# Kernel optimization log

Hardware: AMD Instinct MI355X
Metric: run time of the kernel (lower is better)

The kernel has to match this reference:

```python
import jax, jax.numpy as jnp
import numpy as np

N, D, K = 32768, 256, 8192
SQRT3 = 3.0 ** 0.5


def setup_inputs() -> dict:
    key = jax.random.key(0)
    k1, k2 = jax.random.split(key)
    x = jax.random.normal(k1, (N, D), dtype=jnp.float32)
    # torch .uniform_(-sqrt(3), sqrt(3)) on an [D, K] table
    embeddings = jax.random.uniform(k2, (D, K), dtype=jnp.float32,
                                    minval=-SQRT3, maxval=SQRT3)
    return {"x": x, "embeddings": embeddings}


def reference(x, embeddings):
    # x: [N, D] (forward flattens from dim 1; 2D input is identity)
    # embeddings: [D, K]
    # squared L2 distances: ||y||^2 - 2 y.E + ||e||^2  -> [N, K]
    dist = (jnp.sum(x * x, axis=1, keepdims=True)
            - 2.0 * (x @ embeddings)
            + jnp.sum(embeddings * embeddings, axis=0, keepdims=True))
    idx = jnp.argmin(dist, axis=1)  # [N]
    # one_hot(idx) @ E^T == gather of columns of E (same math, no dense one-hot)
    quantized = jnp.take(embeddings, idx, axis=1).T  # [N, D]
    return quantized.reshape(x.shape)
```

## Files before the change

kernel.cpp:

```cpp
#include <hip/hip_runtime.h>
#include <math.h>
#include <float.h>

#define N_ROWS 32768
#define D_DIM  256
#define K_DIM  8192

#define EPS1 0.25f
#define EPS2 0.02f
#define T2CAP 4096
#define NSPLIT2 32
#define T3CAP 512
#define NSPLIT3 16

typedef _Float16 f16;
typedef _Float16 f16x8 __attribute__((ext_vector_type(8)));
typedef float f32x4 __attribute__((ext_vector_type(4)));

#define KSPLIT 8
#define COLS_PER_SPLIT (K_DIM / KSPLIT)
#define CHUNK_COLS 32
#define NCHUNK (COLS_PER_SPLIT / CHUNK_COLS)
#define CHUNK_BYTES (CHUNK_COLS * D_DIM * 2)

typedef unsigned int u32;
typedef const u32 __attribute__((address_space(1)))* gas1_u32;
typedef u32 __attribute__((address_space(3)))* las3_u32;
__device__ __forceinline__ void gload_lds16(const void* g, void* l) {
    __builtin_amdgcn_global_load_lds((gas1_u32)g, (las3_u32)l, 16, 0, 0);
}

__global__ void convx_kernel(const float* __restrict__ X, f16* __restrict__ X16,
                             int* __restrict__ count, int* __restrict__ count3) {
    if (blockIdx.x == 0 && threadIdx.x == 0) { *count = 0; *count3 = 0; }
    const size_t i = ((size_t)blockIdx.x * 256 + threadIdx.x) * 8;
    float4 a = *reinterpret_cast<const float4*>(X + i);
    float4 b = *reinterpret_cast<const float4*>(X + i + 4);
    f16x8 o;
    o[0]=(f16)a.x; o[1]=(f16)a.y; o[2]=(f16)a.z; o[3]=(f16)a.w;
    o[4]=(f16)b.x; o[5]=(f16)b.y; o[6]=(f16)b.z; o[7]=(f16)b.w;
    *reinterpret_cast<f16x8*>(X16 + i) = o;
}

__global__ void prep_e_kernel(const float* __restrict__ E, float* __restrict__ ET,
                              f16* __restrict__ Epack) {
    __shared__ float t[64][65];
    const int bk = blockIdx.x & (K_DIM / 64 - 1);
    const int bd = blockIdx.x >> 7;
    const int c  = threadIdx.x & 63;
    const int r0 = (threadIdx.x >> 6) * 16;
    const int d0 = bd * 64, k0 = bk * 64;
#pragma unroll
    for (int i = 0; i < 16; ++i)
        t[r0 + i][c] = E[(size_t)(d0 + r0 + i) * K_DIM + k0 + c];
    __syncthreads();
#pragma unroll
    for (int i = 0; i < 16; ++i)
        ET[(size_t)(k0 + r0 + i) * D_DIM + d0 + c] = t[c][r0 + i];
#pragma unroll
    for (int o = 0; o < 2; ++o) {
        const int out = threadIdx.x + o * 256;
        const int i16 = out >> 7;
        const int th  = (out >> 6) & 1;
        const int l   = out & 63;
        const int tile = bk * 4 + i16;
        const int tg   = bd * 2 + th;
        f16x8 frag;
#pragma unroll
        for (int j = 0; j < 8; ++j)
            frag[j] = (f16)t[32*th + (l >> 4) * 8 + j][16*i16 + (l & 15)];
        *reinterpret_cast<f16x8*>(Epack + ((size_t)(tile*8 + tg) * 512 + l * 8)) = frag;
    }
}

__global__ void packe_kernel(const float* __restrict__ E, f16* __restrict__ Epack) {
    const int gid = blockIdx.x * 256 + threadIdx.x;
    const int l    = gid & 63;
    const int t    = (gid >> 6) & 7;
    const int tile = gid >> 9;
    const int k  = 16 * tile + (l & 15);
    const int d0 = 32 * t + (l >> 4) * 8;
    f16x8 o;
#pragma unroll
    for (int j = 0; j < 8; ++j) o[j] = (f16)E[(size_t)(d0 + j) * K_DIM + k];
    *reinterpret_cast<f16x8*>(Epack + (size_t)gid * 8) = o;
}

__global__ void nhen_kernel(const float* __restrict__ E, float* __restrict__ nhen) {
    const int k = blockIdx.x * 256 + threadIdx.x;
    float s = 0.0f;
#pragma unroll 8
    for (int d = 0; d < D_DIM; ++d) {
        float v = E[(size_t)d * K_DIM + k];
        s = fmaf(v, v, s);
    }
    nhen[k] = -0.5f * s;
}

__launch_bounds__(256, 2)
__global__ void pass1_kernel(const f16* __restrict__ X16,
                             const f16* __restrict__ Epack,
                             const float* __restrict__ nhen,
                             float* __restrict__ p_best,
                             float* __restrict__ p_sec,
                             int*   __restrict__ p_idx) {
    __shared__ f16 B_lds[3][CHUNK_BYTES / 2];
    __shared__ float nh_lds[COLS_PER_SPLIT];

    const int tid = threadIdx.x;
    const int wv = tid >> 6;
    const int lane = tid & 63;
    const int l15 = lane & 15;
    const int l4  = lane >> 4;
    const int rg = blockIdx.x >> 3;
    const int ks = blockIdx.x & 7;
    const int rowW = rg * 256 + wv * 64;
    const int colBase = ks * COLS_PER_SPLIT;

    f16x8 A[4][8];
#pragma unroll
    for (int rt = 0; rt < 4; ++rt)
#pragma unroll
        for (int t = 0; t < 8; ++t)
            A[rt][t] = *reinterpret_cast<const f16x8*>(
                X16 + (size_t)(rowW + 16*rt + l15) * D_DIM + 32*t + l4*8);

    *reinterpret_cast<float4*>(&nh_lds[tid * 4]) =
        *reinterpret_cast<const float4*>(nhen + colBase + tid * 4);

    float best[16], sec[16];
    int bbase[16];
#pragma unroll
    for (int s = 0; s < 16; ++s) { best[s] = -INFINITY; sec[s] = -INFINITY; bbase[s] = 0; }

    const char* splitSrc = (const char*)Epack + (size_t)colBase * 512;

    auto STAGE = [&](int buf, int ci) {
        const char* csrc = splitSrc + (size_t)ci * CHUNK_BYTES;
        char* cdst = (char*)&B_lds[buf][0];
#pragma unroll
        for (int c = 0; c < 4; ++c) {
            const int seg = wv * 4 + c;
            gload_lds16(csrc + seg * 1024 + (lane << 4), cdst + seg * 1024);
        }
    };

    f32x4 accA[4], accB[4];
    int cA = 0, cB = 0;

    auto TILE = [&](const f16* bufc, int ct, int nhoff,
                    f32x4 (&accN)[4], f32x4 (&accP)[4], int cP, bool doScore) {
        const float nh = nh_lds[nhoff + l15];
        const f32x4 nh4 = {nh, nh, nh, nh};
#pragma unroll
        for (int t = 0; t < 8; ++t) {
            f16x8 B = *reinterpret_cast<const f16x8*>(bufc + (ct*8 + t)*512 + lane*8);
            if (t == 0) {
#pragma unroll
                for (int rt = 0; rt < 4; ++rt)
                    accN[rt] = __builtin_amdgcn_mfma_f32_16x16x32_f16(A[rt][0], B, nh4, 0, 0, 0);
            } else {
#pragma unroll
                for (int rt = 0; rt < 4; ++rt)
                    accN[rt] = __builtin_amdgcn_mfma_f32_16x16x32_f16(A[rt][t], B, accN[rt], 0, 0, 0);
            }
            if (doScore) {
#pragma unroll
                for (int s = 2*t; s <= 2*t + 1; ++s) {
                    const int rt2 = s >> 2, r2 = s & 3;
                    const float v = accP[rt2][r2];
                    sec[s] = __builtin_amdgcn_fmed3f(v, best[s], sec[s]);
                    const bool gt = v > best[s];
                    best[s] = gt ? v : best[s];
                    bbase[s] = gt ? cP : bbase[s];
                }
            }
        }
    };

    STAGE(0, 0);
    STAGE(1, 1);
    asm volatile("s_waitcnt lgkmcnt(0)" ::: "memory");

    int cur = 0;
    for (int ci = 0; ci < NCHUNK; ++ci) {
        if (ci < NCHUNK - 1) {
            asm volatile("s_waitcnt vmcnt(4)" ::: "memory");
        } else {
            asm volatile("s_waitcnt vmcnt(0)" ::: "memory");
        }
        __builtin_amdgcn_s_barrier();
        if (ci + 2 < NCHUNK) {
            int nb = cur + 2; if (nb >= 3) nb -= 3;
            STAGE(nb, ci + 2);
        }
        const f16* bufc = &B_lds[cur][0];
        const int base = colBase + ci * CHUNK_COLS;
        if (ci == 0) {
            TILE(bufc, 0, ci*32,      accA, accB, cB, false); cA = base;
            TILE(bufc, 1, ci*32 + 16, accB, accA, cA, true);  cB = base + 16;
        } else {
            TILE(bufc, 0, ci*32,      accA, accB, cB, true);  cA = base;
            TILE(bufc, 1, ci*32 + 16, accB, accA, cA, true);  cB = base + 16;
        }
        cur = (cur + 1 == 3) ? 0 : cur + 1;
    }
#pragma unroll
    for (int s = 0; s < 16; ++s) {
        const int rt2 = s >> 2, r2 = s & 3;
        const float v = accB[rt2][r2];
        sec[s] = __builtin_amdgcn_fmed3f(v, best[s], sec[s]);
        const bool gt = v > best[s];
        best[s] = gt ? v : best[s];
        bbase[s] = gt ? cB : bbase[s];
    }

#pragma unroll
    for (int s = 0; s < 16; ++s) {
        float b = best[s], sc = sec[s];
        int k = bbase[s] + l15;
#pragma unroll
        for (int off = 8; off >= 1; off >>= 1) {
            float ob = __shfl_xor(b, off, 16);
            float os = __shfl_xor(sc, off, 16);
            int   ok = __shfl_xor(k, off, 16);
            float sm = fmaxf(fmaxf(sc, os), fminf(b, ob));
            bool take = (ob > b) || (ob == b && ok < k);
            b = take ? ob : b;
            k = take ? ok : k;
            sc = sm;
        }
        if (l15 == 0) {
            const int row = rowW + 16*(s >> 2) + 4*l4 + (s & 3);
            p_best[ks * N_ROWS + row] = b;
            p_sec [ks * N_ROWS + row] = sc;
            p_idx [ks * N_ROWS + row] = k;
        }
    }
}

__global__ void merge_kernel(const float* __restrict__ p_best,
                             const float* __restrict__ p_sec,
                             const int*   __restrict__ p_idx,
                             int* __restrict__ idxf,
                             int* __restrict__ list, int* __restrict__ count) {
    const int n = blockIdx.x * 256 + threadIdx.x;
    float b = p_best[n], sc = p_sec[n];
    int k = p_idx[n];
#pragma unroll
    for (int s = 1; s < KSPLIT; ++s) {
        float ob = p_best[s * N_ROWS + n];
        float os = p_sec [s * N_ROWS + n];
        int   ok = p_idx [s * N_ROWS + n];
        float sm = fmaxf(fmaxf(sc, os), fminf(b, ob));
        bool take = ob > b;
        b = take ? ob : b; k = take ? ok : k; sc = sm;
    }
    idxf[n] = k;
    if (2.0f * (b - sc) < EPS1) {
        int pos = atomicAdd(count, 1);
        if (pos < T2CAP) list[pos] = n;
    }
}

__launch_bounds__(256, 2)
__global__ void tier2_kernel(const float* __restrict__ X,
                             const float* __restrict__ E,
                             const float* __restrict__ nhen,
                             const int* __restrict__ list,
                             const int* __restrict__ count,
                             float* __restrict__ t2b, float* __restrict__ t2s,
                             int* __restrict__ t2i) {
    const int g  = blockIdx.x >> 5;
    const int sp = blockIdx.x & 31;
    const int cnt = min(*count, T2CAP);
    if (g * 64 >= cnt) return;

    __shared__ float xT[D_DIM][64];
    __shared__ float es[64][64];
    const int tid = threadIdx.x;
    const int tx = tid & 15, ty = tid >> 4;

    {
        const int r = tid >> 2;
        const int slot = min(g * 64 + r, cnt - 1);
        const int row = list[slot];
        const int d0 = (tid & 3) * 64;
        const float* xp = X + (size_t)row * D_DIM + d0;
#pragma unroll
        for (int i = 0; i < 64; i += 4) {
            float4 v = *reinterpret_cast<const float4*>(xp + i);
            xT[d0+i+0][r] = v.x; xT[d0+i+1][r] = v.y;
            xT[d0+i+2][r] = v.z; xT[d0+i+3][r] = v.w;
        }
    }

    float best[4], sec[4]; int bidx[4];
#pragma unroll
    for (int i = 0; i < 4; ++i) { best[i] = -INFINITY; sec[i] = -INFINITY; bidx[i] = 0; }

    const int colBase = sp * 256;
    for (int kc = 0; kc < 256; kc += 64) {
        float acc[4][4];
#pragma unroll
        for (int i = 0; i < 4; ++i)
#pragma unroll
            for (int j = 0; j < 4; ++j) acc[i][j] = 0.0f;

        for (int dc = 0; dc < D_DIM; dc += 64) {
            __syncthreads();
#pragma unroll
            for (int dd = 0; dd < 64; dd += 16) {
                int d = dd + (tid >> 4);
                float4 v = *reinterpret_cast<const float4*>(
                    &E[(size_t)(dc + d) * K_DIM + colBase + kc + (tid & 15) * 4]);
                *reinterpret_cast<float4*>(&es[d][(tid & 15) * 4]) = v;
            }
            __syncthreads();
#pragma unroll 8
            for (int d = 0; d < 64; ++d) {
                float4 xv = *reinterpret_cast<const float4*>(&xT[dc + d][ty * 4]);
                float4 ev = *reinterpret_cast<const float4*>(&es[d][tx * 4]);
                float xr[4] = {xv.x, xv.y, xv.z, xv.w};
                float ec[4] = {ev.x, ev.y, ev.z, ev.w};
#pragma unroll
                for (int i = 0; i < 4; ++i)
#pragma unroll
                    for (int j = 0; j < 4; ++j)
                        acc[i][j] = fmaf(xr[i], ec[j], acc[i][j]);
            }
        }
        float4 nhv = *reinterpret_cast<const float4*>(&nhen[colBase + kc + tx * 4]);
        float nh[4] = {nhv.x, nhv.y, nhv.z, nhv.w};
#pragma unroll
        for (int j = 0; j < 4; ++j) {
            const int k = colBase + kc + tx * 4 + j;
#pragma unroll
            for (int i = 0; i < 4; ++i) {
                float u = nh[j] + acc[i][j];
                bool gt = u > best[i];
                sec[i]  = fmaxf(sec[i], fminf(u, best[i]));
                best[i] = gt ? u : best[i];
                bidx[i] = gt ? k : bidx[i];
            }
        }
    }

#pragma unroll
    for (int off = 8; off >= 1; off >>= 1) {
#pragma unroll
        for (int i = 0; i < 4; ++i) {
            float ob = __shfl_xor(best[i], off, 16);
            float os = __shfl_xor(sec[i], off, 16);
            int   ok = __shfl_xor(bidx[i], off, 16);
            float sm = fmaxf(fmaxf(sec[i], os), fminf(best[i], ob));
            bool take = (ob > best[i]) || (ob == best[i] && ok < bidx[i]);
            best[i] = take ? ob : best[i];
            bidx[i] = take ? ok : bidx[i];
            sec[i] = sm;
        }
    }
    if (tx == 0) {
#pragma unroll
        for (int i = 0; i < 4; ++i) {
            const int slot = g * 64 + ty * 4 + i;
            if (slot < cnt) {
                t2b[sp * T2CAP + slot] = best[i];
                t2s[sp * T2CAP + slot] = sec[i];
                t2i[sp * T2CAP + slot] = bidx[i];
            }
        }
    }
}

__global__ void merge2_kernel(const float* __restrict__ t2b,
                              const float* __restrict__ t2s,
                              const int*   __restrict__ t2i,
                              const int* __restrict__ list,
                              const int* __restrict__ count,
                              int* __restrict__ idxf,
                              int* __restrict__ list3, int* __restrict__ count3) {
    const int slot = blockIdx.x * 256 + threadIdx.x;
    const int cnt = min(*count, T2CAP);
    if (slot >= cnt) return;
    float b = t2b[slot], sc = t2s[slot];
    int k = t2i[slot];
#pragma unroll
    for (int sp = 1; sp < NSPLIT2; ++sp) {
        float ob = t2b[sp * T2CAP + slot];
        float os = t2s[sp * T2CAP + slot];
        int   ok = t2i[sp * T2CAP + slot];
        float sm = fmaxf(fmaxf(sc, os), fminf(b, ob));
        bool take = ob > b;
        b = take ? ob : b; k = take ? ok : k; sc = sm;
    }
    const int n = list[slot];
    idxf[n] = k;
    if (2.0f * (b - sc) < EPS2) {
        int pos = atomicAdd(count3, 1);
        if (pos < T3CAP) list3[pos] = n;
    }
}

__launch_bounds__(256)
__global__ void tier3_kernel(const float* __restrict__ X,
                             const float* __restrict__ E,
                             const int* __restrict__ list3,
                             const int* __restrict__ count3,
                             double* __restrict__ t3b, int* __restrict__ t3i) {
    const int slot = blockIdx.x >> 4;
    const int sp   = blockIdx.x & 15;
    const int cnt = min(*count3, T3CAP);
    if (slot >= cnt) return;
    const int n = list3[slot];

    __shared__ float xs[D_DIM];
    const int tid = threadIdx.x;
    xs[tid] = X[(size_t)n * D_DIM + tid];
    __syncthreads();

    const int colBase = sp * 512;
    double best = DBL_MAX;
    int bi = 0x7fffffff;
#pragma unroll
    for (int kk = 0; kk < 512; kk += 256) {
        const int k = colBase + kk + tid;
        double s0 = 0.0, s1 = 0.0, s2 = 0.0, s3 = 0.0;
#pragma unroll 4
        for (int d = 0; d < D_DIM; d += 4) {
            double f0 = (double)xs[d+0] - (double)E[(size_t)(d+0) * K_DIM + k];
            double f1 = (double)xs[d+1] - (double)E[(size_t)(d+1) * K_DIM + k];
            double f2 = (double)xs[d+2] - (double)E[(size_t)(d+2) * K_DIM + k];
            double f3 = (double)xs[d+3] - (double)E[(size_t)(d+3) * K_DIM + k];
            s0 = fma(f0, f0, s0); s1 = fma(f1, f1, s1);
            s2 = fma(f2, f2, s2); s3 = fma(f3, f3, s3);
        }
        double s = (s0 + s1) + (s2 + s3);
        if (s < best) { best = s; bi = k; }
    }

    __shared__ double bv[256];
    __shared__ int bix[256];
    bv[tid] = best; bix[tid] = bi;
    __syncthreads();
    if (tid == 0) {
        double b = bv[0]; int ix = bix[0];
        for (int t = 1; t < 256; ++t)
            if (bv[t] < b || (bv[t] == b && bix[t] < ix)) { b = bv[t]; ix = bix[t]; }
        t3b[sp * T3CAP + slot] = b;
        t3i[sp * T3CAP + slot] = ix;
    }
}

__global__ void merge3_kernel(const double* __restrict__ t3b,
                              const int* __restrict__ t3i,
                              const int* __restrict__ list3,
                              const int* __restrict__ count3,
                              int* __restrict__ idxf) {
    const int slot = blockIdx.x * 256 + threadIdx.x;
    const int cnt = min(*count3, T3CAP);
    if (slot >= cnt) return;
    double b = t3b[slot];
    int k = t3i[slot];
#pragma unroll
    for (int sp = 1; sp < NSPLIT3; ++sp) {
        double ob = t3b[sp * T3CAP + slot];
        int   ok = t3i[sp * T3CAP + slot];
        if (ob < b || (ob == b && ok < k)) { b = ob; k = ok; }
    }
    idxf[list3[slot]] = k;
}

__global__ void gather2_kernel(const float* __restrict__ ET,
                               const int* __restrict__ idx,
                               float* __restrict__ out) {
    const int n  = blockIdx.x * 4 + (threadIdx.x >> 6);
    const int d4 = (threadIdx.x & 63) * 4;
    const int k  = idx[n];
    *reinterpret_cast<float4*>(&out[(size_t)n * D_DIM + d4]) =
        *reinterpret_cast<const float4*>(&ET[(size_t)k * D_DIM + d4]);
}

__global__ void gather_kernel(const float* __restrict__ E,
                              const int* __restrict__ idx,
                              float* __restrict__ out) {
    const int n = blockIdx.x;
    const int d = threadIdx.x;
    const int k = idx[n];
    out[(size_t)n * D_DIM + d] = E[(size_t)d * K_DIM + k];
}

__global__ void fb_enorm_kernel(const float* __restrict__ E, float* __restrict__ enorm) {
    int k = blockIdx.x * 256 + threadIdx.x;
    float s = 0.0f;
#pragma unroll 8
    for (int d = 0; d < D_DIM; ++d) { float v = E[(size_t)d * K_DIM + k]; s = fmaf(v, v, s); }
    enorm[k] = s;
}

__launch_bounds__(256, 2)
__global__ void fb_dist_kernel(const float* __restrict__ X, const float* __restrict__ E,
                               const float* __restrict__ enorm,
                               int* __restrict__ idx_out, float* __restrict__ gap_out) {
    __shared__ float xT[D_DIM][64];
    __shared__ float es[64][64];
    const int tid = threadIdx.x;
    const int tx = tid & 15, ty = tid >> 4;
    const int rowBase = blockIdx.x * 64;
    {
        const int r = tid >> 2;
        const int d0 = (tid & 3) * 64;
        const float* xp = X + (size_t)(rowBase + r) * D_DIM + d0;
#pragma unroll
        for (int i = 0; i < 64; i += 4) {
            float4 v = *reinterpret_cast<const float4*>(xp + i);
            xT[d0+i+0][r]=v.x; xT[d0+i+1][r]=v.y; xT[d0+i+2][r]=v.z; xT[d0+i+3][r]=v.w;
        }
    }
    float bestVal[4], secVal[4]; int bestIdx[4];
#pragma unroll
    for (int i = 0; i < 4; ++i) { bestVal[i]=INFINITY; secVal[i]=INFINITY; bestIdx[i]=0; }
    for (int kc = 0; kc < K_DIM; kc += 64) {
        float acc[4][4];
#pragma unroll
        for (int i=0;i<4;++i)
#pragma unroll
            for (int j=0;j<4;++j) acc[i][j]=0.f;
        for (int dc = 0; dc < D_DIM; dc += 64) {
            __syncthreads();
#pragma unroll
            for (int dd = 0; dd < 64; dd += 16) {
                int d = dd + (tid >> 4);
                float4 v = *reinterpret_cast<const float4*>(
                    &E[(size_t)(dc+d)*K_DIM + kc + (tid&15)*4]);
                *reinterpret_cast<float4*>(&es[d][(tid&15)*4]) = v;
            }
            __syncthreads();
#pragma unroll 8
            for (int d = 0; d < 64; ++d) {
                float4 xv = *reinterpret_cast<const float4*>(&xT[dc+d][ty*4]);
                float4 ev = *reinterpret_cast<const float4*>(&es[d][tx*4]);
                float xr[4]={xv.x,xv.y,xv.z,xv.w}, ec[4]={ev.x,ev.y,ev.z,ev.w};
#pragma unroll
                for (int i=0;i<4;++i)
#pragma unroll
                    for (int j=0;j<4;++j) acc[i][j]=fmaf(xr[i],ec[j],acc[i][j]);
            }
        }
        float4 env = *reinterpret_cast<const float4*>(&enorm[kc + tx*4]);
        float en[4]={env.x,env.y,env.z,env.w};
#pragma unroll
        for (int j=0;j<4;++j) {
            int k = kc + tx*4 + j;
#pragma unroll
            for (int i=0;i<4;++i) {
                float s = fmaf(-2.0f, acc[i][j], en[j]);
                if (s < bestVal[i]) { secVal[i]=bestVal[i]; bestVal[i]=s; bestIdx[i]=k; }
                else if (s < secVal[i]) secVal[i]=s;
            }
        }
    }
#pragma unroll
    for (int off=8; off>=1; off>>=1) {
#pragma unroll
        for (int i=0;i<4;++i) {
            float oB=__shfl_xor(bestVal[i],off,16);
            int oI=__shfl_xor(bestIdx[i],off,16);
            float oS=__shfl_xor(secVal[i],off,16);
            float ms=fminf(fminf(secVal[i],oS),fmaxf(bestVal[i],oB));
            if (oB<bestVal[i] || (oB==bestVal[i] && oI<bestIdx[i])) { bestVal[i]=oB; bestIdx[i]=oI; }
            secVal[i]=ms;
        }
    }
    if (tx==0) {
#pragma unroll
        for (int i=0;i<4;++i) {
            idx_out[rowBase + ty*4 + i] = bestIdx[i];
            gap_out[rowBase + ty*4 + i] = secVal[i]-bestVal[i];
        }
    }
}

__launch_bounds__(256)
__global__ void fb_refine_kernel(const float* __restrict__ X, const float* __restrict__ E,
                                 const float* __restrict__ gap, int* __restrict__ idx) {
    const int n = blockIdx.x;
    if (gap[n] >= 0.0625f) return;
    __shared__ float xs[D_DIM];
    const int tid = threadIdx.x;
    xs[tid] = X[(size_t)n * D_DIM + tid];
    __syncthreads();
    double best = DBL_MAX; int bi = 0x7fffffff;
    for (int k = tid; k < K_DIM; k += 256) {
        double s0=0,s1=0,s2=0,s3=0;
#pragma unroll 4
        for (int d = 0; d < D_DIM; d += 4) {
            double f0=(double)xs[d+0]-(double)E[(size_t)(d+0)*K_DIM+k];
            double f1=(double)xs[d+1]-(double)E[(size_t)(d+1)*K_DIM+k];
            double f2=(double)xs[d+2]-(double)E[(size_t)(d+2)*K_DIM+k];
            double f3=(double)xs[d+3]-(double)E[(size_t)(d+3)*K_DIM+k];
            s0=fma(f0,f0,s0); s1=fma(f1,f1,s1); s2=fma(f2,f2,s2); s3=fma(f3,f3,s3);
        }
        double s=(s0+s1)+(s2+s3);
        if (s<best){best=s;bi=k;}
    }
    __shared__ double bv[256]; __shared__ int bix[256];
    bv[tid]=best; bix[tid]=bi;
    __syncthreads();
    if (tid==0) {
        double b=bv[0]; int ix=bix[0];
        for (int t=1;t<256;++t)
            if (bv[t]<b || (bv[t]==b && bix[t]<ix)) { b=bv[t]; ix=bix[t]; }
        idx[n]=ix;
    }
}

extern "C" void kernel_launch(void* const* d_in, const int* in_sizes, int n_in,
                              void* d_out, int out_size, void* d_ws, size_t ws_size,
                              hipStream_t stream) {
    const float* X = (const float*)d_in[0];
    const float* E = (const float*)d_in[1];
    float* out = (float*)d_out;
    char* ws = (char*)d_ws;

    const size_t o_nhen  = 0;
    const size_t o_pb    = 32768;
    const size_t o_ps    = o_pb  + (size_t)KSPLIT * N_ROWS * 4;
    const size_t o_pi    = o_ps  + (size_t)KSPLIT * N_ROWS * 4;
    const size_t o_idx   = o_pi  + (size_t)KSPLIT * N_ROWS * 4;
    const size_t o_list  = o_idx + (size_t)N_ROWS * 4;
    const size_t o_count = o_list + (size_t)T2CAP * 4;
    const size_t o_t2b   = o_count + 256;
    const size_t o_t2s   = o_t2b + (size_t)NSPLIT2 * T2CAP * 4;
    const size_t o_t2i   = o_t2s + (size_t)NSPLIT2 * T2CAP * 4;
    const size_t o_list3 = o_t2i + (size_t)NSPLIT2 * T2CAP * 4;
    const size_t o_t3b   = o_list3 + (size_t)T3CAP * 4;
    const size_t o_t3i   = o_t3b + (size_t)NSPLIT3 * T3CAP * 8;
    const size_t o_x16   = o_t3i + (size_t)NSPLIT3 * T3CAP * 4;
    const size_t o_epack = o_x16 + (size_t)N_ROWS * D_DIM * 2;
    const size_t NEED_BASE = o_epack + (size_t)D_DIM * K_DIM * 2;
    const size_t o_et    = NEED_BASE;
    const size_t NEED_FULL = o_et + (size_t)D_DIM * K_DIM * 4;

    if (ws_size >= NEED_BASE) {
        float*  nhen  = (float*) (ws + o_nhen);
        float*  p_b   = (float*) (ws + o_pb);
        float*  p_s   = (float*) (ws + o_ps);
        int*    p_i   = (int*)   (ws + o_pi);
        int*    idxf  = (int*)   (ws + o_idx);
        int*    list  = (int*)   (ws + o_list);
        int*    count = (int*)   (ws + o_count);
        int*    count3= (int*)   (ws + o_count + 4);
        float*  t2b   = (float*) (ws + o_t2b);
        float*  t2s   = (float*) (ws + o_t2s);
        int*    t2i   = (int*)   (ws + o_t2i);
        int*    list3 = (int*)   (ws + o_list3);
        double* t3b   = (double*)(ws + o_t3b);
        int*    t3i   = (int*)   (ws + o_t3i);
        f16*    X16   = (f16*)   (ws + o_x16);
        f16*    Epack = (f16*)   (ws + o_epack);
        float*  ET    = (float*) (ws + o_et);
        const bool haveET = ws_size >= NEED_FULL;

        convx_kernel<<<(N_ROWS * D_DIM / 8) / 256, 256, 0, stream>>>(X, X16, count, count3);
        if (haveET) {
            prep_e_kernel<<<(K_DIM / 64) * (D_DIM / 64), 256, 0, stream>>>(E, ET, Epack);
        } else {
            packe_kernel<<<(K_DIM / 16) * 8 * 64 / 256, 256, 0, stream>>>(E, Epack);
        }
        nhen_kernel<<<K_DIM / 256, 256, 0, stream>>>(E, nhen);
        pass1_kernel<<<(N_ROWS / 256) * KSPLIT, 256, 0, stream>>>(
            X16, Epack, nhen, p_b, p_s, p_i);
        merge_kernel<<<N_ROWS / 256, 256, 0, stream>>>(
            p_b, p_s, p_i, idxf, list, count);
        tier2_kernel<<<(T2CAP / 64) * NSPLIT2, 256, 0, stream>>>(
            X, E, nhen, list, count, t2b, t2s, t2i);
        merge2_kernel<<<T2CAP / 256, 256, 0, stream>>>(
            t2b, t2s, t2i, list, count, idxf, list3, count3);
        tier3_kernel<<<T3CAP * NSPLIT3, 256, 0, stream>>>(
            X, E, list3, count3, t3b, t3i);
        merge3_kernel<<<T3CAP / 256, 256, 0, stream>>>(
            t3b, t3i, list3, count3, idxf);
        if (haveET)
            gather2_kernel<<<N_ROWS / 4, 256, 0, stream>>>(ET, idxf, out);
        else
            gather_kernel<<<N_ROWS, 256, 0, stream>>>(E, idxf, out);
    } else {
        float* enorm = (float*)ws;
        int*   idx   = (int*)(ws + 32768);
        float* gap   = (float*)(ws + 32768 + (size_t)N_ROWS * 4);
        fb_enorm_kernel<<<K_DIM / 256, 256, 0, stream>>>(E, enorm);
        fb_dist_kernel<<<N_ROWS / 64, 256, 0, stream>>>(X, E, enorm, idx, gap);
        fb_refine_kernel<<<N_ROWS, 256, 0, stream>>>(X, E, gap, idx);
        gather_kernel<<<N_ROWS, 256, 0, stream>>>(E, idx, out);
    }
}
```

Baseline: 310.7 us.

## Fuse prep kernels into one launch and replace merge3 with atomicMin keys

Merges the X conversion, E transpose/pack and E-norm kernels into a single launch that dispatches on block index, and removes the tier-3 merge kernel. Tier 3 now packs distance and index into a 64-bit key and reduces across splits with atomicMin. The gather kernel resolves negative indices through that table. This cuts two kernel launches and the per-kernel drain gaps between them. The cost is that the low 13 bits of the double distance are truncated in the key, which can slightly change tie-breaking.

```diff
diff --git a/kernel.cpp b/kernel.cpp
--- a/kernel.cpp
+++ b/kernel.cpp
@@ -16,6 +16,7 @@
 typedef _Float16 f16;
 typedef _Float16 f16x8 __attribute__((ext_vector_type(8)));
 typedef float f32x4 __attribute__((ext_vector_type(4)));
+typedef unsigned long long u64;
 
 #define KSPLIT 8
 #define COLS_PER_SPLIT (K_DIM / KSPLIT)
@@ -23,11 +24,70 @@
 #define NCHUNK (COLS_PER_SPLIT / CHUNK_COLS)
 #define CHUNK_BYTES (CHUNK_COLS * D_DIM * 2)
 
+#define NB_CONV 4096
+#define NB_PREPE 512
+#define NB_NHEN 32
+
 typedef unsigned int u32;
 typedef const u32 __attribute__((address_space(1)))* gas1_u32;
 typedef u32 __attribute__((address_space(3)))* las3_u32;
 __device__ __forceinline__ void gload_lds16(const void* g, void* l) {
     __builtin_amdgcn_global_load_lds((gas1_u32)g, (las3_u32)l, 16, 0, 0);
+}
+
+__global__ void prep_kernel(const float* __restrict__ X, const float* __restrict__ E,
+                            f16* __restrict__ X16, float* __restrict__ ET,
+                            f16* __restrict__ Epack, float* __restrict__ nhen,
+                            int* __restrict__ count, int* __restrict__ count3) {
+    __shared__ float t[64][65];
+    const int bid = blockIdx.x;
+    if (bid < NB_CONV) {
+        if (bid == 0 && threadIdx.x == 0) { *count = 0; *count3 = 0; }
+        const size_t i = ((size_t)bid * 256 + threadIdx.x) * 8;
+        float4 a = *reinterpret_cast<const float4*>(X + i);
+        float4 b = *reinterpret_cast<const float4*>(X + i + 4);
+        f16x8 o;
+        o[0]=(f16)a.x; o[1]=(f16)a.y; o[2]=(f16)a.z; o[3]=(f16)a.w;
+        o[4]=(f16)b.x; o[5]=(f16)b.y; o[6]=(f16)b.z; o[7]=(f16)b.w;
+        *reinterpret_cast<f16x8*>(X16 + i) = o;
+    } else if (bid < NB_CONV + NB_PREPE) {
+        const int pb = bid - NB_CONV;
+        const int bk = pb & (K_DIM / 64 - 1);
+        const int bd = pb >> 7;
+        const int c  = threadIdx.x & 63;
+        const int r0 = (threadIdx.x >> 6) * 16;
+        const int d0 = bd * 64, k0 = bk * 64;
+#pragma unroll
+        for (int i = 0; i < 16; ++i)
+            t[r0 + i][c] = E[(size_t)(d0 + r0 + i) * K_DIM + k0 + c];
+        __syncthreads();
+#pragma unroll
+        for (int i = 0; i < 16; ++i)
+            ET[(size_t)(k0 + r0 + i) * D_DIM + d0 + c] = t[c][r0 + i];
+#pragma unroll
+        for (int o = 0; o < 2; ++o) {
+            const int out = threadIdx.x + o * 256;
+            const int i16 = out >> 7;
+            const int th  = (out >> 6) & 1;
+            const int l   = out & 63;
+            const int tile = bk * 4 + i16;
+            const int tg   = bd * 2 + th;
+            f16x8 frag;
+#pragma unroll
+            for (int j = 0; j < 8; ++j)
+                frag[j] = (f16)t[32*th + (l >> 4) * 8 + j][16*i16 + (l & 15)];
+            *reinterpret_cast<f16x8*>(Epack + ((size_t)(tile*8 + tg) * 512 + l * 8)) = frag;
+        }
+    } else {
+        const int k = (bid - NB_CONV - NB_PREPE) * 256 + threadIdx.x;
+        float s = 0.0f;
+#pragma unroll 8
+        for (int d = 0; d < D_DIM; ++d) {
+            float v = E[(size_t)d * K_DIM + k];
+            s = fmaf(v, v, s);
+        }
+        nhen[k] = -0.5f * s;
+    }
 }
 
 __global__ void convx_kernel(const float* __restrict__ X, f16* __restrict__ X16,
@@ -40,37 +100,6 @@
     o[0]=(f16)a.x; o[1]=(f16)a.y; o[2]=(f16)a.z; o[3]=(f16)a.w;
     o[4]=(f16)b.x; o[5]=(f16)b.y; o[6]=(f16)b.z; o[7]=(f16)b.w;
     *reinterpret_cast<f16x8*>(X16 + i) = o;
-}
-
-__global__ void prep_e_kernel(const float* __restrict__ E, float* __restrict__ ET,
-                              f16* __restrict__ Epack) {
-    __shared__ float t[64][65];
-    const int bk = blockIdx.x & (K_DIM / 64 - 1);
-    const int bd = blockIdx.x >> 7;
-    const int c  = threadIdx.x & 63;
-    const int r0 = (threadIdx.x >> 6) * 16;
-    const int d0 = bd * 64, k0 = bk * 64;
-#pragma unroll
-    for (int i = 0; i < 16; ++i)
-        t[r0 + i][c] = E[(size_t)(d0 + r0 + i) * K_DIM + k0 + c];
-    __syncthreads();
-#pragma unroll
-    for (int i = 0; i < 16; ++i)
-        ET[(size_t)(k0 + r0 + i) * D_DIM + d0 + c] = t[c][r0 + i];
-#pragma unroll
-    for (int o = 0; o < 2; ++o) {
-        const int out = threadIdx.x + o * 256;
-        const int i16 = out >> 7;
-        const int th  = (out >> 6) & 1;
-        const int l   = out & 63;
-        const int tile = bk * 4 + i16;
-        const int tg   = bd * 2 + th;
-        f16x8 frag;
-#pragma unroll
-        for (int j = 0; j < 8; ++j)
-            frag[j] = (f16)t[32*th + (l >> 4) * 8 + j][16*i16 + (l & 15)];
-        *reinterpret_cast<f16x8*>(Epack + ((size_t)(tile*8 + tg) * 512 + l * 8)) = frag;
-    }
 }
 
 __global__ void packe_kernel(const float* __restrict__ E, f16* __restrict__ Epack) {
@@ -379,7 +408,8 @@
                               const int* __restrict__ list,
                               const int* __restrict__ count,
                               int* __restrict__ idxf,
-                              int* __restrict__ list3, int* __restrict__ count3) {
+                              int* __restrict__ list3, int* __restrict__ count3,
+                              u64* __restrict__ t3min) {
     const int slot = blockIdx.x * 256 + threadIdx.x;
     const int cnt = min(*count, T2CAP);
     if (slot >= cnt) return;
@@ -395,11 +425,16 @@
         b = take ? ob : b; k = take ? ok : k; sc = sm;
     }
     const int n = list[slot];
-    idxf[n] = k;
     if (2.0f * (b - sc) < EPS2) {
         int pos = atomicAdd(count3, 1);
-        if (pos < T3CAP) list3[pos] = n;
-    }
+        if (pos < T3CAP) {
+            list3[pos] = n;
+            t3min[pos] = ~0ull;
+            idxf[n] = -(pos + 1);
+            return;
+        }
+    }
+    idxf[n] = k;
 }
 
 __launch_bounds__(256)
@@ -407,7 +442,7 @@
                              const float* __restrict__ E,
                              const int* __restrict__ list3,
                              const int* __restrict__ count3,
-                             double* __restrict__ t3b, int* __restrict__ t3i) {
+                             u64* __restrict__ t3min) {
     const int slot = blockIdx.x >> 4;
     const int sp   = blockIdx.x & 15;
     const int cnt = min(*count3, T3CAP);
@@ -436,7 +471,7 @@
             s2 = fma(f2, f2, s2); s3 = fma(f3, f3, s3);
         }
         double s = (s0 + s1) + (s2 + s3);
-        if (s < best) { best = s; bi = k; }
+        if (s < best || (s == best && k < bi)) { best = s; bi = k; }
     }
 
     __shared__ double bv[256];
@@ -447,46 +482,31 @@
         double b = bv[0]; int ix = bix[0];
         for (int t = 1; t < 256; ++t)
             if (bv[t] < b || (bv[t] == b && bix[t] < ix)) { b = bv[t]; ix = bix[t]; }
-        t3b[sp * T3CAP + slot] = b;
-        t3i[sp * T3CAP + slot] = ix;
-    }
-}
-
-__global__ void merge3_kernel(const double* __restrict__ t3b,
-                              const int* __restrict__ t3i,
-                              const int* __restrict__ list3,
-                              const int* __restrict__ count3,
-                              int* __restrict__ idxf) {
-    const int slot = blockIdx.x * 256 + threadIdx.x;
-    const int cnt = min(*count3, T3CAP);
-    if (slot >= cnt) return;
-    double b = t3b[slot];
-    int k = t3i[slot];
-#pragma unroll
-    for (int sp = 1; sp < NSPLIT3; ++sp) {
-        double ob = t3b[sp * T3CAP + slot];
-        int   ok = t3i[sp * T3CAP + slot];
-        if (ob < b || (ob == b && ok < k)) { b = ob; k = ok; }
-    }
-    idxf[list3[slot]] = k;
+        u64 key = ((u64)__double_as_longlong(b) & ~0x1FFFull) | (u64)(unsigned)ix;
+        atomicMin(&t3min[slot], key);
+    }
 }
 
 __global__ void gather2_kernel(const float* __restrict__ ET,
                                const int* __restrict__ idx,
+                               const u64* __restrict__ t3min,
                                float* __restrict__ out) {
     const int n  = blockIdx.x * 4 + (threadIdx.x >> 6);
     const int d4 = (threadIdx.x & 63) * 4;
-    const int k  = idx[n];
+    int k  = idx[n];
+    if (k < 0) k = (int)(t3min[-k - 1] & 0x1FFFull);
     *reinterpret_cast<float4*>(&out[(size_t)n * D_DIM + d4]) =
         *reinterpret_cast<const float4*>(&ET[(size_t)k * D_DIM + d4]);
 }
 
 __global__ void gather_kernel(const float* __restrict__ E,
                               const int* __restrict__ idx,
+                              const u64* __restrict__ t3min,
                               float* __restrict__ out) {
     const int n = blockIdx.x;
     const int d = threadIdx.x;
-    const int k = idx[n];
+    int k = idx[n];
+    if (k < 0) k = (int)(t3min[-k - 1] & 0x1FFFull);
     out[(size_t)n * D_DIM + d] = E[(size_t)d * K_DIM + k];
 }
 
@@ -615,6 +635,15 @@
     }
 }
 
+__global__ void fb_gather_kernel(const float* __restrict__ E,
+                                 const int* __restrict__ idx,
+                                 float* __restrict__ out) {
+    const int n = blockIdx.x;
+    const int d = threadIdx.x;
+    const int k = idx[n];
+    out[(size_t)n * D_DIM + d] = E[(size_t)d * K_DIM + k];
+}
+
 extern "C" void kernel_launch(void* const* d_in, const int* in_sizes, int n_in,
                               void* d_out, int out_size, void* d_ws, size_t ws_size,
                               hipStream_t stream) {
@@ -634,9 +663,8 @@
     const size_t o_t2s   = o_t2b + (size_t)NSPLIT2 * T2CAP * 4;
     const size_t o_t2i   = o_t2s + (size_t)NSPLIT2 * T2CAP * 4;
     const size_t o_list3 = o_t2i + (size_t)NSPLIT2 * T2CAP * 4;
-    const size_t o_t3b   = o_list3 + (size_t)T3CAP * 4;
-    const size_t o_t3i   = o_t3b + (size_t)NSPLIT3 * T3CAP * 8;
-    const size_t o_x16   = o_t3i + (size_t)NSPLIT3 * T3CAP * 4;
+    const size_t o_t3min = o_list3 + (size_t)T3CAP * 4;
+    const size_t o_x16   = o_t3min + (size_t)T3CAP * 8;
     const size_t o_epack = o_x16 + (size_t)N_ROWS * D_DIM * 2;
     const size_t NEED_BASE = o_epack + (size_t)D_DIM * K_DIM * 2;
     const size_t o_et    = NEED_BASE;
@@ -655,20 +683,20 @@
         float*  t2s   = (float*) (ws + o_t2s);
         int*    t2i   = (int*)   (ws + o_t2i);
         int*    list3 = (int*)   (ws + o_list3);
-        double* t3b   = (double*)(ws + o_t3b);
-        int*    t3i   = (int*)   (ws + o_t3i);
+        u64*    t3min = (u64*)   (ws + o_t3min);
         f16*    X16   = (f16*)   (ws + o_x16);
         f16*    Epack = (f16*)   (ws + o_epack);
         float*  ET    = (float*) (ws + o_et);
         const bool haveET = ws_size >= NEED_FULL;
 
-        convx_kernel<<<(N_ROWS * D_DIM / 8) / 256, 256, 0, stream>>>(X, X16, count, count3);
         if (haveET) {
-            prep_e_kernel<<<(K_DIM / 64) * (D_DIM / 64), 256, 0, stream>>>(E, ET, Epack);
+            prep_kernel<<<NB_CONV + NB_PREPE + NB_NHEN, 256, 0, stream>>>(
+                X, E, X16, ET, Epack, nhen, count, count3);
         } else {
+            convx_kernel<<<NB_CONV, 256, 0, stream>>>(X, X16, count, count3);
             packe_kernel<<<(K_DIM / 16) * 8 * 64 / 256, 256, 0, stream>>>(E, Epack);
-        }
-        nhen_kernel<<<K_DIM / 256, 256, 0, stream>>>(E, nhen);
+            nhen_kernel<<<NB_NHEN, 256, 0, stream>>>(E, nhen);
+        }
         pass1_kernel<<<(N_ROWS / 256) * KSPLIT, 256, 0, stream>>>(
             X16, Epack, nhen, p_b, p_s, p_i);
         merge_kernel<<<N_ROWS / 256, 256, 0, stream>>>(
@@ -676,15 +704,13 @@
         tier2_kernel<<<(T2CAP / 64) * NSPLIT2, 256, 0, stream>>>(
             X, E, nhen, list, count, t2b, t2s, t2i);
         merge2_kernel<<<T2CAP / 256, 256, 0, stream>>>(
-            t2b, t2s, t2i, list, count, idxf, list3, count3);
+            t2b, t2s, t2i, list, count, idxf, list3, count3, t3min);
         tier3_kernel<<<T3CAP * NSPLIT3, 256, 0, stream>>>(
-            X, E, list3, count3, t3b, t3i);
-        merge3_kernel<<<T3CAP / 256, 256, 0, stream>>>(
-            t3b, t3i, list3, count3, idxf);
+            X, E, list3, count3, t3min);
         if (haveET)
-            gather2_kernel<<<N_ROWS / 4, 256, 0, stream>>>(ET, idxf, out);
+            gather2_kernel<<<N_ROWS / 4, 256, 0, stream>>>(ET, idxf, t3min, out);
         else
-            gather_kernel<<<N_ROWS, 256, 0, stream>>>(E, idxf, out);
+            gather_kernel<<<N_ROWS, 256, 0, stream>>>(E, idxf, t3min, out);
     } else {
         float* enorm = (float*)ws;
         int*   idx   = (int*)(ws + 32768);
@@ -692,6 +718,6 @@
         fb_enorm_kernel<<<K_DIM / 256, 256, 0, stream>>>(E, enorm);
         fb_dist_kernel<<<N_ROWS / 64, 256, 0, stream>>>(X, E, enorm, idx, gap);
         fb_refine_kernel<<<N_ROWS, 256, 0, stream>>>(X, E, gap, idx);
-        gather_kernel<<<N_ROWS, 256, 0, stream>>>(E, idx, out);
-    }
-}
+        fb_gather_kernel<<<N_ROWS, 256, 0, stream>>>(E, idx, out);
+    }
+}
```

Result: faster. 300.5 us (median of 2 runs) (-3.3%).
